# Kernel optimization log

Measured on AMD Instinct MI355X. Metric: run time of the kernel, lower is better.

Reference implementation:

```python
import jax, jax.numpy as jnp
import numpy as np

NU = NI = 100_000  # nodes per ntype
E = 500_000        # edges per metapath graph
M = 2              # metapaths per ntype
D = 64             # in_size == out_size (num_heads = 1)
H = 128            # semantic-attention hidden
B = 8192           # batch of (user, pos, neg) indices
LRELU = 0.2        # DGL GATConv leaky-relu slope
EPS = 1e-5


def setup_inputs() -> dict:
    key = jax.random.key(0)
    ks = iter(jax.random.split(key, 40))
    rn = lambda sh, s=0.1: jax.random.normal(next(ks), sh, jnp.float32) * s
    ri = lambda sh, hi: jax.random.randint(next(ks), sh, 0, hi, jnp.int32)
    return dict(
        user_idx=ri((B,), NU), item_idx=ri((B,), NI), neg_item_idx=ri((B,), NI),
        user_feat=rn((NU, D), 1.0), item_feat=rn((NI, D), 1.0),
        u_src=ri((M, E), NU), u_dst=ri((M, E), NU),
        i_src=ri((M, E), NI), i_dst=ri((M, E), NI),
        u_W=rn((M, D, D)), u_al=rn((M, D)), u_ar=rn((M, D)), u_b=rn((M, D)),
        i_W=rn((M, D, D)), i_al=rn((M, D)), i_ar=rn((M, D)), i_b=rn((M, D)),
        u_saW1=rn((D, H)), u_sab1=rn((H,)), u_saW2=rn((H, 1)),
        i_saW1=rn((D, H)), i_sab1=rn((H,)), i_saW2=rn((H, 1)),
        userW=rn((D, D)), userb=rn((D,)), itemW=rn((D, D)), itemb=rn((D,)),
        ln_g=jnp.ones((D,), jnp.float32), ln_b=jnp.zeros((D,), jnp.float32),
    )


def _gat_stack(h, W, al, ar, b, src, dst, n_nodes):
    # One GATConv (single head) per metapath, vmapped over the metapath axis.
    def one(Wm, alm, arm, bm, s, d):
        feat = h @ Wm                               # (N, D)
        el = feat @ alm                             # (N,)
        er = feat @ arm                             # (N,)
        e = jax.nn.leaky_relu(el[s] + er[d], LRELU)  # (E,)
        m = jax.ops.segment_max(e, d, num_segments=n_nodes)
        ex = jnp.exp(e - m[d])
        den = jax.ops.segment_sum(ex, d, num_segments=n_nodes)
        alpha = ex / (den[d] + 1e-9)                # per-dst edge softmax
        out = jax.ops.segment_sum(alpha[:, None] * feat[s], d, num_segments=n_nodes)
        return jax.nn.elu(out + bm)                 # (N, D)
    return jax.vmap(one)(W, al, ar, b, src, dst)    # (M, N, D)


def _semantic_attention(z, W1, b1, W2):
    # z: (M, N, D) -> (N, D)
    w = jnp.mean(jnp.tanh(jnp.einsum('mnd,dh->mnh', z, W1) + b1) @ W2, axis=1)  # (M, 1)
    beta = jax.nn.softmax(w, axis=0)                 # softmax over metapaths
    return jnp.sum(beta[:, :, None] * z, axis=0)     # (N, D) -- beta (M,1)->(M,1,1)


def _layernorm(x, g, b):
    mu = x.mean(-1, keepdims=True)
    v = ((x - mu) ** 2).mean(-1, keepdims=True)
    return g * (x - mu) / jnp.sqrt(v + EPS) + b


def reference(user_idx, item_idx, neg_item_idx, user_feat, item_feat,
              u_src, u_dst, i_src, i_dst,
              u_W, u_al, u_ar, u_b, i_W, i_al, i_ar, i_b,
              u_saW1, u_sab1, u_saW2, i_saW1, i_sab1, i_saW2,
              userW, userb, itemW, itemb, ln_g, ln_b):
    zu = _gat_stack(user_feat, u_W, u_al, u_ar, u_b, u_src, u_dst, NU)
    zi = _gat_stack(item_feat, i_W, i_al, i_ar, i_b, i_src, i_dst, NI)
    user_emb = _semantic_attention(zu, u_saW1, u_sab1, u_saW2)
    item_emb = _semantic_attention(zi, i_saW1, i_sab1, i_saW2)
    user_emb = _layernorm(jax.nn.relu(user_emb @ userW + userb), ln_g, ln_b)
    item_emb = _layernorm(jax.nn.relu(item_emb @ itemW + itemb), ln_g, ln_b)
    return (user_emb[user_idx], item_emb[item_idx], item_emb[neg_item_idx])
```

## Files before the change

kernel.cpp:

```cpp
#include <hip/hip_runtime.h>
#include <math.h>

#define N_NODES 100000
#define N_EDGES 500000
#define BATCH   8192
#define NBLK    98

typedef __bf16 bf16;
typedef __bf16 bf16x8 __attribute__((ext_vector_type(8)));
typedef float  f32x4  __attribute__((ext_vector_type(4)));

#define MFMA16(a, b, c) __builtin_amdgcn_mfma_f32_16x16x32_bf16((a), (b), (c), 0, 0, 0)

__device__ __forceinline__ float wave_reduce_sum(float v) {
    #pragma unroll
    for (int off = 32; off; off >>= 1) v += __shfl_xor(v, off);
    return v;
}

__device__ __forceinline__ float fast_tanh(float x) {
    float e = __expf(2.f * x);
    return 1.f - 2.f / (e + 1.f);
}

__device__ __forceinline__ float b2f(unsigned short u) {
    return __int_as_float(((int)u) << 16);
}

__global__ void __launch_bounds__(256, 4)
feat_mfma(const float* __restrict__ uf, const float* __restrict__ itf,
          const float* __restrict__ uW, const float* __restrict__ iW,
          const float* __restrict__ ual, const float* __restrict__ ial,
          const float* __restrict__ uar, const float* __restrict__ iar,
          bf16* __restrict__ feat, float* __restrict__ el,
          float* __restrict__ er, int N) {
    const int t = blockIdx.y;
    const float* h   = t ? itf : uf;
    const float* Wb  = t ? iW : uW;
    const float* alb = t ? ial : ual;
    const float* arb = t ? iar : uar;
    __shared__ bf16x8 ldsW[16][64];
    for (int f = threadIdx.x; f < 16 * 64; f += blockDim.x) {
        int id = f >> 6, l = f & 63;
        int lc = l & 15, lq = l >> 4;
        int kf = id & 1, nt = (id >> 1) & 3, m = id >> 3;
        bf16x8 v;
        #pragma unroll
        for (int j = 0; j < 8; ++j)
            v[j] = (bf16)Wb[m * 4096 + (kf * 32 + lq * 8 + j) * 64 + nt * 16 + lc];
        ldsW[id][l] = v;
    }
    __syncthreads();
    const int lane = threadIdx.x & 63, wave = threadIdx.x >> 6, wpb = blockDim.x >> 6;
    const int c = lane & 15, q = lane >> 4;
    float alv[2][4], arv[2][4];
    #pragma unroll
    for (int m = 0; m < 2; ++m)
        #pragma unroll
        for (int nt = 0; nt < 4; ++nt) {
            alv[m][nt] = alb[m * 64 + nt * 16 + c];
            arv[m][nt] = arb[m * 64 + nt * 16 + c];
        }
    const f32x4 zf = {0.f, 0.f, 0.f, 0.f};
    const int tiles = N >> 4;
    for (int tile = blockIdx.x * wpb + wave; tile < tiles; tile += gridDim.x * wpb) {
        const float* hr = h + (size_t)(tile * 16 + c) * 64 + q * 8;
        f32x4 v0 = *(const f32x4*)hr;
        f32x4 v1 = *(const f32x4*)(hr + 4);
        f32x4 v2 = *(const f32x4*)(hr + 32);
        f32x4 v3 = *(const f32x4*)(hr + 36);
        bf16x8 a0, a1;
        #pragma unroll
        for (int j = 0; j < 4; ++j) {
            a0[j] = (bf16)v0[j]; a0[j + 4] = (bf16)v1[j];
            a1[j] = (bf16)v2[j]; a1[j + 4] = (bf16)v3[j];
        }
        #pragma unroll
        for (int m = 0; m < 2; ++m) {
            const int g = t * 2 + m;
            bf16* fg   = feat + (size_t)g * N * 64;
            float* elg = el + (size_t)g * N;
            float* erg = er + (size_t)g * N;
            f32x4 acc[4];
            #pragma unroll
            for (int nt = 0; nt < 4; ++nt) {
                acc[nt] = zf;
                acc[nt] = MFMA16(a0, ldsW[(m * 4 + nt) * 2][lane], acc[nt]);
                acc[nt] = MFMA16(a1, ldsW[(m * 4 + nt) * 2 + 1][lane], acc[nt]);
            }
            #pragma unroll
            for (int nt = 0; nt < 4; ++nt)
                #pragma unroll
                for (int r = 0; r < 4; ++r)
                    fg[(size_t)(tile * 16 + q * 4 + r) * 64 + nt * 16 + c] = (bf16)acc[nt][r];
            #pragma unroll
            for (int r = 0; r < 4; ++r) {
                float se = 0.f, sr = 0.f;
                #pragma unroll
                for (int nt = 0; nt < 4; ++nt) {
                    se = fmaf(acc[nt][r], alv[m][nt], se);
                    sr = fmaf(acc[nt][r], arv[m][nt], sr);
                }
                #pragma unroll
                for (int off = 1; off < 16; off <<= 1) {
                    se += __shfl_xor(se, off);
                    sr += __shfl_xor(sr, off);
                }
                if (c == 0) {
                    elg[tile * 16 + q * 4 + r] = se;
                    erg[tile * 16 + q * 4 + r] = sr;
                }
            }
        }
    }
}

__global__ void hist_all(const int* __restrict__ udst, const int* __restrict__ idst,
                         int* __restrict__ counts, int* __restrict__ rank, int E, int N) {
    const int g = blockIdx.y;
    const int* dst = ((g < 2) ? udst : idst) + (size_t)(g & 1) * E;
    int* cnt = counts + (size_t)g * N;
    int* rk  = rank + (size_t)g * E;
    for (int i = blockIdx.x * blockDim.x + threadIdx.x; i < E; i += gridDim.x * blockDim.x)
        rk[i] = atomicAdd(&cnt[dst[i]], 1);
}

__global__ void scanA(const int* __restrict__ counts, int* __restrict__ offsets,
                      int* __restrict__ bsum, int N) {
    const int g = blockIdx.y;
    const int* c = counts + (size_t)g * N;
    int* o = offsets + (size_t)g * (N + 1);
    __shared__ int sh[1024];
    int i = blockIdx.x * 1024 + (int)threadIdx.x;
    int v = (i < N) ? c[i] : 0;
    sh[threadIdx.x] = v;
    __syncthreads();
    for (int off = 1; off < 1024; off <<= 1) {
        int tv = (threadIdx.x >= (unsigned)off) ? sh[threadIdx.x - off] : 0;
        __syncthreads();
        sh[threadIdx.x] += tv;
        __syncthreads();
    }
    if (i < N) o[i] = sh[threadIdx.x] - v;
    if (threadIdx.x == 1023) bsum[g * 128 + blockIdx.x] = sh[1023];
}

__global__ void scanB(int* __restrict__ bsum, int* __restrict__ offsets, int N) {
    const int g = blockIdx.y;
    int* bs = bsum + g * 128;
    __shared__ int sh[128];
    int tid = (int)threadIdx.x;
    int v = (tid < NBLK) ? bs[tid] : 0;
    sh[tid] = v;
    __syncthreads();
    for (int off = 1; off < 128; off <<= 1) {
        int tv = (tid >= off) ? sh[tid - off] : 0;
        __syncthreads();
        sh[tid] += tv;
        __syncthreads();
    }
    if (tid < NBLK) bs[tid] = sh[tid] - v;
    if (tid == 0) offsets[(size_t)g * (N + 1) + N] = sh[127];
}

__global__ void scanC(int* __restrict__ offsets, const int* __restrict__ bsum, int N) {
    const int g = blockIdx.y;
    int i = blockIdx.x * blockDim.x + threadIdx.x;
    if (i < N)
        offsets[(size_t)g * (N + 1) + i] += bsum[g * 128 + (i >> 10)];
}

__global__ void scatter_all(const int* __restrict__ usrc, const int* __restrict__ udst,
                            const int* __restrict__ isrc, const int* __restrict__ idst,
                            const float* __restrict__ el, const float* __restrict__ er,
                            const int* __restrict__ offsets, const int* __restrict__ rank,
                            int2* __restrict__ epack, int E, int N) {
    const int g = blockIdx.y;
    const int* src = ((g < 2) ? usrc : isrc) + (size_t)(g & 1) * E;
    const int* dst = ((g < 2) ? udst : idst) + (size_t)(g & 1) * E;
    const float* elg = el + (size_t)g * N;
    const float* erg = er + (size_t)g * N;
    const int* offg = offsets + (size_t)g * (N + 1);
    const int* rk = rank + (size_t)g * E;
    int2* ep = epack + (size_t)g * E;
    for (int i = blockIdx.x * blockDim.x + threadIdx.x; i < E; i += gridDim.x * blockDim.x) {
        int s = src[i], d = dst[i];
        int pos = offg[d] + rk[i];
        float e = elg[s] + erg[d];
        e = (e >= 0.f) ? e : 0.2f * e;
        float w = __expf(e);
        ep[pos] = make_int2(s << 7, __float_as_int(w));
    }
}

__global__ void agg_all(const unsigned short* __restrict__ feat,
                        const float* __restrict__ ub, const float* __restrict__ ib,
                        const int* __restrict__ offsets, const int2* __restrict__ epack,
                        bf16* __restrict__ z, int E, int N) {
    const int g = blockIdx.y;
    const char* featg = (const char*)(feat + (size_t)g * N * 64);
    const float* bv = ((g < 2) ? ub : ib) + (g & 1) * 64;
    const int* offg = offsets + (size_t)g * (N + 1);
    const int2* ep = epack + (size_t)g * E;
    bf16* zg = z + (size_t)g * N * 64;
    const int lane = threadIdx.x & 63, wave = threadIdx.x >> 6, wpb = blockDim.x >> 6;
    const int lane2 = lane * 2;
    const float bl = bv[lane];
    for (int node0 = blockIdx.x * wpb + wave; node0 < N; node0 += gridDim.x * wpb) {
        const int node = __builtin_amdgcn_readfirstlane(node0);
        const int beg = __builtin_amdgcn_readfirstlane(offg[node]);
        const int end = __builtin_amdgcn_readfirstlane(offg[node + 1]);
        float l = 0.f, acc0 = 0.f, acc1 = 0.f;
        int i = beg;
        for (; i + 4 <= end; i += 4) {
            int2 p0 = ep[i], p1 = ep[i + 1], p2 = ep[i + 2], p3 = ep[i + 3];
            float f0 = b2f(*(const unsigned short*)(featg + (p0.x + lane2)));
            float f1 = b2f(*(const unsigned short*)(featg + (p1.x + lane2)));
            float f2 = b2f(*(const unsigned short*)(featg + (p2.x + lane2)));
            float f3 = b2f(*(const unsigned short*)(featg + (p3.x + lane2)));
            float w0 = __int_as_float(p0.y), w1 = __int_as_float(p1.y);
            float w2 = __int_as_float(p2.y), w3 = __int_as_float(p3.y);
            l += (w0 + w1) + (w2 + w3);
            acc0 = fmaf(w0, f0, acc0);
            acc1 = fmaf(w1, f1, acc1);
            acc0 = fmaf(w2, f2, acc0);
            acc1 = fmaf(w3, f3, acc1);
        }
        for (; i < end; ++i) {
            int2 p = ep[i];
            float w = __int_as_float(p.y);
            l += w;
            acc0 = fmaf(w, b2f(*(const unsigned short*)(featg + (p.x + lane2))), acc0);
        }
        float acc = acc0 + acc1;
        float o = acc / (l + 1e-9f);
        float zz = o + bl;
        zz = (zz > 0.f) ? zz : expm1f(zz);
        zg[(size_t)node * 64 + lane] = (bf16)zz;
    }
}

__global__ void __launch_bounds__(256, 4)
sem_mfma(const bf16* __restrict__ z,
         const float* __restrict__ uW1, const float* __restrict__ iW1,
         const float* __restrict__ ub1, const float* __restrict__ ib1,
         const float* __restrict__ uW2, const float* __restrict__ iW2,
         float* __restrict__ wsum, int N) {
    const int g = blockIdx.y, t = g >> 1;
    const float* W1 = t ? iW1 : uW1;
    const float* b1 = t ? ib1 : ub1;
    const float* W2 = t ? iW2 : uW2;
    __shared__ bf16x8 ldsW[16][64];
    for (int f = threadIdx.x; f < 16 * 64; f += blockDim.x) {
        int id = f >> 6, l = f & 63;
        int lc = l & 15, lq = l >> 4;
        int nt = id >> 1, kf = id & 1;
        bf16x8 v;
        #pragma unroll
        for (int j = 0; j < 8; ++j)
            v[j] = (bf16)W1[(kf * 32 + lq * 8 + j) * 128 + nt * 16 + lc];
        ldsW[id][l] = v;
    }
    __syncthreads();
    const int lane = threadIdx.x & 63, wave = threadIdx.x >> 6, wpb = blockDim.x >> 6;
    const int c = lane & 15, q = lane >> 4;
    float b1v[8], w2v[8];
    #pragma unroll
    for (int nt = 0; nt < 8; ++nt) { b1v[nt] = b1[nt * 16 + c]; w2v[nt] = W2[nt * 16 + c]; }
    const bf16* zg = z + (size_t)g * N * 64;
    const f32x4 zf = {0.f, 0.f, 0.f, 0.f};
    float local = 0.f;
    const int tiles = N >> 4;
    for (int tile = blockIdx.x * wpb + wave; tile < tiles; tile += gridDim.x * wpb) {
        const bf16* zr = zg + (size_t)(tile * 16 + c) * 64;
        bf16x8 a0 = *(const bf16x8*)(zr + q * 8);
        bf16x8 a1 = *(const bf16x8*)(zr + 32 + q * 8);
        f32x4 acc[8];
        #pragma unroll
        for (int nt = 0; nt < 8; ++nt) {
            acc[nt] = zf;
            acc[nt] = MFMA16(a0, ldsW[nt * 2][lane], acc[nt]);
            acc[nt] = MFMA16(a1, ldsW[nt * 2 + 1][lane], acc[nt]);
        }
        #pragma unroll
        for (int nt = 0; nt < 8; ++nt)
            #pragma unroll
            for (int r = 0; r < 4; ++r)
                local += w2v[nt] * fast_tanh(acc[nt][r] + b1v[nt]);
    }
    local = wave_reduce_sum(local);
    if (lane == 0) atomicAdd(&wsum[g], local);
}

__global__ void out_all(const int* __restrict__ uidx, const int* __restrict__ iidx,
                        const int* __restrict__ nidx, const bf16* __restrict__ z,
                        const float* __restrict__ wsum,
                        const float* __restrict__ userW, const float* __restrict__ userb,
                        const float* __restrict__ itemW, const float* __restrict__ itemb,
                        const float* __restrict__ ln_g, const float* __restrict__ ln_b,
                        float* __restrict__ out, int N, int B) {
    const int grp = blockIdx.y;
    const int t = (grp == 0) ? 0 : 1;
    const float* Wt = t ? itemW : userW;
    const float* bt = t ? itemb : userb;
    const int* idx = (grp == 0) ? uidx : ((grp == 1) ? iidx : nidx);
    const bf16* zg = z + (size_t)(t * 2) * N * 64;
    const int lane = threadIdx.x & 63, wave = threadIdx.x >> 6, wpb = blockDim.x >> 6;
    float Wc[64];
    #pragma unroll
    for (int k = 0; k < 64; ++k) Wc[k] = Wt[k * 64 + lane];
    const float btl = bt[lane], gl = ln_g[lane], lbl = ln_b[lane];
    const float invN = 1.f / (float)N;
    float w0 = wsum[t * 2] * invN, w1 = wsum[t * 2 + 1] * invN;
    float mx = fmaxf(w0, w1);
    float e0 = __expf(w0 - mx), e1 = __expf(w1 - mx);
    float bsum = e0 + e1;
    float beta0 = e0 / bsum, beta1 = e1 / bsum;
    for (int r = blockIdx.x * wpb + wave; r < B; r += gridDim.x * wpb) {
        const int urr = __builtin_amdgcn_readfirstlane(r);
        const int un = __builtin_amdgcn_readfirstlane(idx[urr]);
        float e = beta0 * (float)zg[(size_t)un * 64 + lane]
                + beta1 * (float)zg[(size_t)(N + un) * 64 + lane];
        float y = btl;
        #pragma unroll
        for (int k = 0; k < 64; ++k) y = fmaf(__shfl(e, k), Wc[k], y);
        y = fmaxf(y, 0.f);
        float mu = wave_reduce_sum(y) * (1.f / 64.f);
        float d = y - mu;
        float var = wave_reduce_sum(d * d) * (1.f / 64.f);
        out[(size_t)(grp * B + r) * 64 + lane] = gl * d / sqrtf(var + 1e-5f) + lbl;
    }
}

extern "C" void kernel_launch(void* const* d_in, const int* in_sizes, int n_in,
                              void* d_out, int out_size, void* d_ws, size_t ws_size,
                              hipStream_t stream) {
    const int* user_idx = (const int*)d_in[0];
    const int* item_idx = (const int*)d_in[1];
    const int* neg_idx  = (const int*)d_in[2];
    const float* user_feat = (const float*)d_in[3];
    const float* item_feat = (const float*)d_in[4];
    const int* u_src = (const int*)d_in[5];
    const int* u_dst = (const int*)d_in[6];
    const int* i_src = (const int*)d_in[7];
    const int* i_dst = (const int*)d_in[8];
    const float* u_W  = (const float*)d_in[9];
    const float* u_al = (const float*)d_in[10];
    const float* u_ar = (const float*)d_in[11];
    const float* u_b  = (const float*)d_in[12];
    const float* i_W  = (const float*)d_in[13];
    const float* i_al = (const float*)d_in[14];
    const float* i_ar = (const float*)d_in[15];
    const float* i_b  = (const float*)d_in[16];
    const float* u_saW1 = (const float*)d_in[17];
    const float* u_sab1 = (const float*)d_in[18];
    const float* u_saW2 = (const float*)d_in[19];
    const float* i_saW1 = (const float*)d_in[20];
    const float* i_sab1 = (const float*)d_in[21];
    const float* i_saW2 = (const float*)d_in[22];
    const float* userW = (const float*)d_in[23];
    const float* userb = (const float*)d_in[24];
    const float* itemW = (const float*)d_in[25];
    const float* itemb = (const float*)d_in[26];
    const float* ln_g  = (const float*)d_in[27];
    const float* ln_b  = (const float*)d_in[28];

    const int N = N_NODES, E = N_EDGES, B = BATCH;

    char* ws = (char*)d_ws;
    size_t off = 0;
    auto alloc = [&](size_t bytes) -> char* {
        char* p = ws + off;
        off += (bytes + 255) & ~(size_t)255;
        return p;
    };
    bf16* feat   = (bf16*)alloc((size_t)4 * N * 64 * 2);
    bf16* z      = (bf16*)alloc((size_t)4 * N * 64 * 2);
    float* el    = (float*)alloc((size_t)4 * N * 4);
    float* er    = (float*)alloc((size_t)4 * N * 4);
    int* offsets = (int*)alloc((size_t)4 * (N + 1) * 4);
    int* counts  = (int*)alloc((size_t)4 * N * 4);
    int* rank    = (int*)alloc((size_t)4 * E * 4);
    int2* epack  = (int2*)alloc((size_t)4 * E * 8);
    int* bsum    = (int*)alloc((size_t)4 * 128 * 4);
    float* wsum  = (float*)alloc(16);
    (void)ws_size; (void)in_sizes; (void)n_in; (void)out_size;

    dim3 blk(256);
    hipMemsetAsync(wsum, 0, 16, stream);
    hipMemsetAsync(counts, 0, (size_t)4 * N * 4, stream);

    feat_mfma<<<dim3(256, 2), blk, 0, stream>>>(user_feat, item_feat, u_W, i_W,
                                                u_al, i_al, u_ar, i_ar, feat, el, er, N);
    hist_all<<<dim3(512, 4), blk, 0, stream>>>(u_dst, i_dst, counts, rank, E, N);
    scanA<<<dim3(NBLK, 4), dim3(1024), 0, stream>>>(counts, offsets, bsum, N);
    scanB<<<dim3(1, 4), dim3(128), 0, stream>>>(bsum, offsets, N);
    scanC<<<dim3(391, 4), blk, 0, stream>>>(offsets, bsum, N);
    scatter_all<<<dim3(1024, 4), blk, 0, stream>>>(u_src, u_dst, i_src, i_dst,
                                                   el, er, offsets, rank, epack, E, N);
    agg_all<<<dim3(2048, 4), blk, 0, stream>>>((const unsigned short*)feat, u_b, i_b,
                                               offsets, epack, z, E, N);
    sem_mfma<<<dim3(256, 4), blk, 0, stream>>>(z, u_saW1, i_saW1, u_sab1, i_sab1,
                                               u_saW2, i_saW2, wsum, N);
    out_all<<<dim3(512, 3), blk, 0, stream>>>(user_idx, item_idx, neg_idx, z, wsum,
                                              userW, userb, itemW, itemb, ln_g, ln_b,
                                              (float*)d_out, N, B);
}
```

Measured before the change: 352.5 us.

## Split degree histogram into four sub-counters and aggregate four nodes per wave

The histogram now spreads its atomics over four sub-count arrays chosen by edge index, to reduce atomic contention. The scan sums the four sub-counts, and scanC writes per-node int4 sub-offsets that the scatter uses to place edges. Scatter and histogram are unrolled by four for more loads in flight. Aggregation has each wave handle four consecutive nodes in lockstep up to the largest of their degrees, to expose more independent gathers; the cost is padded iterations and a larger zeroing memset.

Result: slower. 378.1 us (+7.3%).

```diff
diff --git a/kernel.cpp b/kernel.cpp
--- a/kernel.cpp
+++ b/kernel.cpp
@@ -116,23 +116,41 @@
 }
 
 __global__ void hist_all(const int* __restrict__ udst, const int* __restrict__ idst,
-                         int* __restrict__ counts, int* __restrict__ rank, int E, int N) {
+                         int* __restrict__ cnt4, int* __restrict__ rank, int E, int N) {
     const int g = blockIdx.y;
     const int* dst = ((g < 2) ? udst : idst) + (size_t)(g & 1) * E;
-    int* cnt = counts + (size_t)g * N;
-    int* rk  = rank + (size_t)g * E;
-    for (int i = blockIdx.x * blockDim.x + threadIdx.x; i < E; i += gridDim.x * blockDim.x)
-        rk[i] = atomicAdd(&cnt[dst[i]], 1);
-}
-
-__global__ void scanA(const int* __restrict__ counts, int* __restrict__ offsets,
+    int* cntg = cnt4 + (size_t)g * N;
+    int* rk = rank + (size_t)g * E;
+    const int tid = blockIdx.x * blockDim.x + threadIdx.x;
+    const int stride = gridDim.x * blockDim.x;
+    for (int i0 = tid; i0 < E; i0 += 4 * stride) {
+        const int i1 = i0 + stride, i2 = i0 + 2 * stride, i3 = i0 + 3 * stride;
+        int d0 = dst[i0];
+        int d1 = (i1 < E) ? dst[i1] : 0;
+        int d2 = (i2 < E) ? dst[i2] : 0;
+        int d3 = (i3 < E) ? dst[i3] : 0;
+        int r0 = 0, r1 = 0, r2 = 0, r3 = 0;
+        r0 = atomicAdd(&cntg[(size_t)(i0 & 3) * 4 * N + d0], 1);
+        if (i1 < E) r1 = atomicAdd(&cntg[(size_t)(i1 & 3) * 4 * N + d1], 1);
+        if (i2 < E) r2 = atomicAdd(&cntg[(size_t)(i2 & 3) * 4 * N + d2], 1);
+        if (i3 < E) r3 = atomicAdd(&cntg[(size_t)(i3 & 3) * 4 * N + d3], 1);
+        rk[i0] = r0;
+        if (i1 < E) rk[i1] = r1;
+        if (i2 < E) rk[i2] = r2;
+        if (i3 < E) rk[i3] = r3;
+    }
+}
+
+__global__ void scanA(const int* __restrict__ cnt4, int* __restrict__ offsets,
                       int* __restrict__ bsum, int N) {
     const int g = blockIdx.y;
-    const int* c = counts + (size_t)g * N;
+    const int* c = cnt4 + (size_t)g * N;
     int* o = offsets + (size_t)g * (N + 1);
     __shared__ int sh[1024];
     int i = blockIdx.x * 1024 + (int)threadIdx.x;
-    int v = (i < N) ? c[i] : 0;
+    int v = 0;
+    if (i < N)
+        v = c[i] + c[(size_t)4 * N + i] + c[(size_t)8 * N + i] + c[(size_t)12 * N + i];
     sh[threadIdx.x] = v;
     __syncthreads();
     for (int off = 1; off < 1024; off <<= 1) {
@@ -163,33 +181,48 @@
     if (tid == 0) offsets[(size_t)g * (N + 1) + N] = sh[127];
 }
 
-__global__ void scanC(int* __restrict__ offsets, const int* __restrict__ bsum, int N) {
+__global__ void scanC(int* __restrict__ offsets, int* __restrict__ off4,
+                      const int* __restrict__ cnt4, const int* __restrict__ bsum, int N) {
     const int g = blockIdx.y;
     int i = blockIdx.x * blockDim.x + threadIdx.x;
-    if (i < N)
-        offsets[(size_t)g * (N + 1) + i] += bsum[g * 128 + (i >> 10)];
+    if (i < N) {
+        int base = offsets[(size_t)g * (N + 1) + i] + bsum[g * 128 + (i >> 10)];
+        offsets[(size_t)g * (N + 1) + i] = base;
+        const int* c = cnt4 + (size_t)g * N;
+        int c0 = c[i], c1 = c[(size_t)4 * N + i], c2 = c[(size_t)8 * N + i];
+        int4 o;
+        o.x = base; o.y = base + c0; o.z = base + c0 + c1; o.w = base + c0 + c1 + c2;
+        *(int4*)(off4 + ((size_t)g * N + i) * 4) = o;
+    }
 }
 
 __global__ void scatter_all(const int* __restrict__ usrc, const int* __restrict__ udst,
                             const int* __restrict__ isrc, const int* __restrict__ idst,
                             const float* __restrict__ el, const float* __restrict__ er,
-                            const int* __restrict__ offsets, const int* __restrict__ rank,
+                            const int* __restrict__ off4, const int* __restrict__ rank,
                             int2* __restrict__ epack, int E, int N) {
     const int g = blockIdx.y;
     const int* src = ((g < 2) ? usrc : isrc) + (size_t)(g & 1) * E;
     const int* dst = ((g < 2) ? udst : idst) + (size_t)(g & 1) * E;
     const float* elg = el + (size_t)g * N;
     const float* erg = er + (size_t)g * N;
-    const int* offg = offsets + (size_t)g * (N + 1);
+    const int* o4 = off4 + (size_t)g * N * 4;
     const int* rk = rank + (size_t)g * E;
     int2* ep = epack + (size_t)g * E;
-    for (int i = blockIdx.x * blockDim.x + threadIdx.x; i < E; i += gridDim.x * blockDim.x) {
-        int s = src[i], d = dst[i];
-        int pos = offg[d] + rk[i];
-        float e = elg[s] + erg[d];
-        e = (e >= 0.f) ? e : 0.2f * e;
-        float w = __expf(e);
-        ep[pos] = make_int2(s << 7, __float_as_int(w));
+    const int tid = blockIdx.x * blockDim.x + threadIdx.x;
+    const int stride = gridDim.x * blockDim.x;
+    for (int i0 = tid; i0 < E; i0 += 4 * stride) {
+        #pragma unroll
+        for (int u = 0; u < 4; ++u) {
+            const int i = i0 + u * stride;
+            if (i < E) {
+                int s = src[i], d = dst[i];
+                int pos = o4[d * 4 + (i & 3)] + rk[i];
+                float e = elg[s] + erg[d];
+                e = (e >= 0.f) ? e : 0.2f * e;
+                ep[pos] = make_int2(s << 7, __float_as_int(__expf(e)));
+            }
+        }
     }
 }
 
@@ -206,37 +239,61 @@
     const int lane = threadIdx.x & 63, wave = threadIdx.x >> 6, wpb = blockDim.x >> 6;
     const int lane2 = lane * 2;
     const float bl = bv[lane];
-    for (int node0 = blockIdx.x * wpb + wave; node0 < N; node0 += gridDim.x * wpb) {
-        const int node = __builtin_amdgcn_readfirstlane(node0);
-        const int beg = __builtin_amdgcn_readfirstlane(offg[node]);
-        const int end = __builtin_amdgcn_readfirstlane(offg[node + 1]);
-        float l = 0.f, acc0 = 0.f, acc1 = 0.f;
-        int i = beg;
-        for (; i + 4 <= end; i += 4) {
-            int2 p0 = ep[i], p1 = ep[i + 1], p2 = ep[i + 2], p3 = ep[i + 3];
-            float f0 = b2f(*(const unsigned short*)(featg + (p0.x + lane2)));
-            float f1 = b2f(*(const unsigned short*)(featg + (p1.x + lane2)));
-            float f2 = b2f(*(const unsigned short*)(featg + (p2.x + lane2)));
-            float f3 = b2f(*(const unsigned short*)(featg + (p3.x + lane2)));
-            float w0 = __int_as_float(p0.y), w1 = __int_as_float(p1.y);
-            float w2 = __int_as_float(p2.y), w3 = __int_as_float(p3.y);
-            l += (w0 + w1) + (w2 + w3);
-            acc0 = fmaf(w0, f0, acc0);
-            acc1 = fmaf(w1, f1, acc1);
-            acc0 = fmaf(w2, f2, acc0);
-            acc1 = fmaf(w3, f3, acc1);
-        }
-        for (; i < end; ++i) {
-            int2 p = ep[i];
-            float w = __int_as_float(p.y);
-            l += w;
-            acc0 = fmaf(w, b2f(*(const unsigned short*)(featg + (p.x + lane2))), acc0);
-        }
-        float acc = acc0 + acc1;
-        float o = acc / (l + 1e-9f);
-        float zz = o + bl;
-        zz = (zz > 0.f) ? zz : expm1f(zz);
-        zg[(size_t)node * 64 + lane] = (bf16)zz;
+    const int nquad = N >> 2;
+    for (int quad = blockIdx.x * wpb + wave; quad < nquad; quad += gridDim.x * wpb) {
+        const int n0 = __builtin_amdgcn_readfirstlane(quad << 2);
+        const int o0 = __builtin_amdgcn_readfirstlane(offg[n0]);
+        const int o1 = __builtin_amdgcn_readfirstlane(offg[n0 + 1]);
+        const int o2 = __builtin_amdgcn_readfirstlane(offg[n0 + 2]);
+        const int o3 = __builtin_amdgcn_readfirstlane(offg[n0 + 3]);
+        const int o4_ = __builtin_amdgcn_readfirstlane(offg[n0 + 4]);
+        const int d0 = o1 - o0, d1 = o2 - o1, d2 = o3 - o2, d3 = o4_ - o3;
+        int maxd = max(max(d0, d1), max(d2, d3));
+        float l0 = 0.f, l1 = 0.f, l2 = 0.f, l3 = 0.f;
+        float a0 = 0.f, a1 = 0.f, a2 = 0.f, a3 = 0.f;
+        for (int s = 0; s < maxd; s += 2) {
+            const int sA = s, sB = s + 1;
+            int2 pA0 = ep[(sA < d0) ? o0 + sA : 0];
+            int2 pA1 = ep[(sA < d1) ? o1 + sA : 0];
+            int2 pA2 = ep[(sA < d2) ? o2 + sA : 0];
+            int2 pA3 = ep[(sA < d3) ? o3 + sA : 0];
+            int2 pB0 = ep[(sB < d0) ? o0 + sB : 0];
+            int2 pB1 = ep[(sB < d1) ? o1 + sB : 0];
+            int2 pB2 = ep[(sB < d2) ? o2 + sB : 0];
+            int2 pB3 = ep[(sB < d3) ? o3 + sB : 0];
+            float fA0 = b2f(*(const unsigned short*)(featg + (pA0.x + lane2)));
+            float fA1 = b2f(*(const unsigned short*)(featg + (pA1.x + lane2)));
+            float fA2 = b2f(*(const unsigned short*)(featg + (pA2.x + lane2)));
+            float fA3 = b2f(*(const unsigned short*)(featg + (pA3.x + lane2)));
+            float fB0 = b2f(*(const unsigned short*)(featg + (pB0.x + lane2)));
+            float fB1 = b2f(*(const unsigned short*)(featg + (pB1.x + lane2)));
+            float fB2 = b2f(*(const unsigned short*)(featg + (pB2.x + lane2)));
+            float fB3 = b2f(*(const unsigned short*)(featg + (pB3.x + lane2)));
+            float wA0 = (sA < d0) ? __int_as_float(pA0.y) : 0.f;
+            float wA1 = (sA < d1) ? __int_as_float(pA1.y) : 0.f;
+            float wA2 = (sA < d2) ? __int_as_float(pA2.y) : 0.f;
+            float wA3 = (sA < d3) ? __int_as_float(pA3.y) : 0.f;
+            float wB0 = (sB < d0) ? __int_as_float(pB0.y) : 0.f;
+            float wB1 = (sB < d1) ? __int_as_float(pB1.y) : 0.f;
+            float wB2 = (sB < d2) ? __int_as_float(pB2.y) : 0.f;
+            float wB3 = (sB < d3) ? __int_as_float(pB3.y) : 0.f;
+            l0 += wA0 + wB0; l1 += wA1 + wB1; l2 += wA2 + wB2; l3 += wA3 + wB3;
+            a0 = fmaf(wA0, fA0, a0); a0 = fmaf(wB0, fB0, a0);
+            a1 = fmaf(wA1, fA1, a1); a1 = fmaf(wB1, fB1, a1);
+            a2 = fmaf(wA2, fA2, a2); a2 = fmaf(wB2, fB2, a2);
+            a3 = fmaf(wA3, fA3, a3); a3 = fmaf(wB3, fB3, a3);
+        }
+        float oo0 = a0 / (l0 + 1e-9f), oo1 = a1 / (l1 + 1e-9f);
+        float oo2 = a2 / (l2 + 1e-9f), oo3 = a3 / (l3 + 1e-9f);
+        float z0 = oo0 + bl, z1 = oo1 + bl, z2 = oo2 + bl, z3 = oo3 + bl;
+        z0 = (z0 > 0.f) ? z0 : expm1f(z0);
+        z1 = (z1 > 0.f) ? z1 : expm1f(z1);
+        z2 = (z2 > 0.f) ? z2 : expm1f(z2);
+        z3 = (z3 > 0.f) ? z3 : expm1f(z3);
+        zg[(size_t)(n0 + 0) * 64 + lane] = (bf16)z0;
+        zg[(size_t)(n0 + 1) * 64 + lane] = (bf16)z1;
+        zg[(size_t)(n0 + 2) * 64 + lane] = (bf16)z2;
+        zg[(size_t)(n0 + 3) * 64 + lane] = (bf16)z3;
     }
 }
 
@@ -379,7 +436,8 @@
     float* el    = (float*)alloc((size_t)4 * N * 4);
     float* er    = (float*)alloc((size_t)4 * N * 4);
     int* offsets = (int*)alloc((size_t)4 * (N + 1) * 4);
-    int* counts  = (int*)alloc((size_t)4 * N * 4);
+    int* cnt4    = (int*)alloc((size_t)16 * N * 4);
+    int* off4    = (int*)alloc((size_t)4 * N * 4 * 4);
     int* rank    = (int*)alloc((size_t)4 * E * 4);
     int2* epack  = (int2*)alloc((size_t)4 * E * 8);
     int* bsum    = (int*)alloc((size_t)4 * 128 * 4);
@@ -388,17 +446,17 @@
 
     dim3 blk(256);
     hipMemsetAsync(wsum, 0, 16, stream);
-    hipMemsetAsync(counts, 0, (size_t)4 * N * 4, stream);
+    hipMemsetAsync(cnt4, 0, (size_t)16 * N * 4, stream);
 
     feat_mfma<<<dim3(256, 2), blk, 0, stream>>>(user_feat, item_feat, u_W, i_W,
                                                 u_al, i_al, u_ar, i_ar, feat, el, er, N);
-    hist_all<<<dim3(512, 4), blk, 0, stream>>>(u_dst, i_dst, counts, rank, E, N);
-    scanA<<<dim3(NBLK, 4), dim3(1024), 0, stream>>>(counts, offsets, bsum, N);
+    hist_all<<<dim3(512, 4), blk, 0, stream>>>(u_dst, i_dst, cnt4, rank, E, N);
+    scanA<<<dim3(NBLK, 4), dim3(1024), 0, stream>>>(cnt4, offsets, bsum, N);
     scanB<<<dim3(1, 4), dim3(128), 0, stream>>>(bsum, offsets, N);
-    scanC<<<dim3(391, 4), blk, 0, stream>>>(offsets, bsum, N);
-    scatter_all<<<dim3(1024, 4), blk, 0, stream>>>(u_src, u_dst, i_src, i_dst,
-                                                   el, er, offsets, rank, epack, E, N);
-    agg_all<<<dim3(2048, 4), blk, 0, stream>>>((const unsigned short*)feat, u_b, i_b,
+    scanC<<<dim3(391, 4), blk, 0, stream>>>(offsets, off4, cnt4, bsum, N);
+    scatter_all<<<dim3(512, 4), blk, 0, stream>>>(u_src, u_dst, i_src, i_dst,
+                                                  el, er, off4, rank, epack, E, N);
+    agg_all<<<dim3(6250, 4), blk, 0, stream>>>((const unsigned short*)feat, u_b, i_b,
                                                offsets, epack, z, E, N);
     sem_mfma<<<dim3(256, 4), blk, 0, stream>>>(z, u_saW1, i_saW1, u_sab1, i_sab1,
                                                u_saW2, i_saW2, wsum, N);
```

## Split per-destination histogram counters into four sub-counters to reduce atomic contention

Applied to the files above, without the earlier changes.

Replaces the single per-node edge counter with four sub-counters selected by edge index mod 4, and unrolls the histogram and scatter loops by four. scanA sums the sub-counters, and scanC emits per-sub-counter base offsets that scatter uses to place edges. This is meant to reduce atomic contention and raise memory-level parallelism in the CSR build. In exchange it adds a 4x larger memset, extra scan reads and an off4 table write, and scatter gathers from a wider table.

Result: slower. 373.2 us (+5.9%).

```diff
diff --git a/kernel.cpp b/kernel.cpp
--- a/kernel.cpp
+++ b/kernel.cpp
@@ -116,23 +116,41 @@
 }
 
 __global__ void hist_all(const int* __restrict__ udst, const int* __restrict__ idst,
-                         int* __restrict__ counts, int* __restrict__ rank, int E, int N) {
+                         int* __restrict__ cnt4, int* __restrict__ rank, int E, int N) {
     const int g = blockIdx.y;
     const int* dst = ((g < 2) ? udst : idst) + (size_t)(g & 1) * E;
-    int* cnt = counts + (size_t)g * N;
-    int* rk  = rank + (size_t)g * E;
-    for (int i = blockIdx.x * blockDim.x + threadIdx.x; i < E; i += gridDim.x * blockDim.x)
-        rk[i] = atomicAdd(&cnt[dst[i]], 1);
-}
-
-__global__ void scanA(const int* __restrict__ counts, int* __restrict__ offsets,
+    int* cntg = cnt4 + (size_t)g * N;
+    int* rk = rank + (size_t)g * E;
+    const int tid = blockIdx.x * blockDim.x + threadIdx.x;
+    const int stride = gridDim.x * blockDim.x;
+    for (int i0 = tid; i0 < E; i0 += 4 * stride) {
+        const int i1 = i0 + stride, i2 = i0 + 2 * stride, i3 = i0 + 3 * stride;
+        int d0 = dst[i0];
+        int d1 = (i1 < E) ? dst[i1] : 0;
+        int d2 = (i2 < E) ? dst[i2] : 0;
+        int d3 = (i3 < E) ? dst[i3] : 0;
+        int r0 = 0, r1 = 0, r2 = 0, r3 = 0;
+        r0 = atomicAdd(&cntg[(size_t)(i0 & 3) * 4 * N + d0], 1);
+        if (i1 < E) r1 = atomicAdd(&cntg[(size_t)(i1 & 3) * 4 * N + d1], 1);
+        if (i2 < E) r2 = atomicAdd(&cntg[(size_t)(i2 & 3) * 4 * N + d2], 1);
+        if (i3 < E) r3 = atomicAdd(&cntg[(size_t)(i3 & 3) * 4 * N + d3], 1);
+        rk[i0] = r0;
+        if (i1 < E) rk[i1] = r1;
+        if (i2 < E) rk[i2] = r2;
+        if (i3 < E) rk[i3] = r3;
+    }
+}
+
+__global__ void scanA(const int* __restrict__ cnt4, int* __restrict__ offsets,
                       int* __restrict__ bsum, int N) {
     const int g = blockIdx.y;
-    const int* c = counts + (size_t)g * N;
+    const int* c = cnt4 + (size_t)g * N;
     int* o = offsets + (size_t)g * (N + 1);
     __shared__ int sh[1024];
     int i = blockIdx.x * 1024 + (int)threadIdx.x;
-    int v = (i < N) ? c[i] : 0;
+    int v = 0;
+    if (i < N)
+        v = c[i] + c[(size_t)4 * N + i] + c[(size_t)8 * N + i] + c[(size_t)12 * N + i];
     sh[threadIdx.x] = v;
     __syncthreads();
     for (int off = 1; off < 1024; off <<= 1) {
@@ -163,33 +181,48 @@
     if (tid == 0) offsets[(size_t)g * (N + 1) + N] = sh[127];
 }
 
-__global__ void scanC(int* __restrict__ offsets, const int* __restrict__ bsum, int N) {
+__global__ void scanC(int* __restrict__ offsets, int* __restrict__ off4,
+                      const int* __restrict__ cnt4, const int* __restrict__ bsum, int N) {
     const int g = blockIdx.y;
     int i = blockIdx.x * blockDim.x + threadIdx.x;
-    if (i < N)
-        offsets[(size_t)g * (N + 1) + i] += bsum[g * 128 + (i >> 10)];
+    if (i < N) {
+        int base = offsets[(size_t)g * (N + 1) + i] + bsum[g * 128 + (i >> 10)];
+        offsets[(size_t)g * (N + 1) + i] = base;
+        const int* c = cnt4 + (size_t)g * N;
+        int c0 = c[i], c1 = c[(size_t)4 * N + i], c2 = c[(size_t)8 * N + i];
+        int4 o;
+        o.x = base; o.y = base + c0; o.z = base + c0 + c1; o.w = base + c0 + c1 + c2;
+        *(int4*)(off4 + ((size_t)g * N + i) * 4) = o;
+    }
 }
 
 __global__ void scatter_all(const int* __restrict__ usrc, const int* __restrict__ udst,
                             const int* __restrict__ isrc, const int* __restrict__ idst,
                             const float* __restrict__ el, const float* __restrict__ er,
-                            const int* __restrict__ offsets, const int* __restrict__ rank,
+                            const int* __restrict__ off4, const int* __restrict__ rank,
                             int2* __restrict__ epack, int E, int N) {
     const int g = blockIdx.y;
     const int* src = ((g < 2) ? usrc : isrc) + (size_t)(g & 1) * E;
     const int* dst = ((g < 2) ? udst : idst) + (size_t)(g & 1) * E;
     const float* elg = el + (size_t)g * N;
     const float* erg = er + (size_t)g * N;
-    const int* offg = offsets + (size_t)g * (N + 1);
+    const int* o4 = off4 + (size_t)g * N * 4;
     const int* rk = rank + (size_t)g * E;
     int2* ep = epack + (size_t)g * E;
-    for (int i = blockIdx.x * blockDim.x + threadIdx.x; i < E; i += gridDim.x * blockDim.x) {
-        int s = src[i], d = dst[i];
-        int pos = offg[d] + rk[i];
-        float e = elg[s] + erg[d];
-        e = (e >= 0.f) ? e : 0.2f * e;
-        float w = __expf(e);
-        ep[pos] = make_int2(s << 7, __float_as_int(w));
+    const int tid = blockIdx.x * blockDim.x + threadIdx.x;
+    const int stride = gridDim.x * blockDim.x;
+    for (int i0 = tid; i0 < E; i0 += 4 * stride) {
+        #pragma unroll
+        for (int u = 0; u < 4; ++u) {
+            const int i = i0 + u * stride;
+            if (i < E) {
+                int s = src[i], d = dst[i];
+                int pos = o4[d * 4 + (i & 3)] + rk[i];
+                float e = elg[s] + erg[d];
+                e = (e >= 0.f) ? e : 0.2f * e;
+                ep[pos] = make_int2(s << 7, __float_as_int(__expf(e)));
+            }
+        }
     }
 }
 
@@ -379,7 +412,8 @@
     float* el    = (float*)alloc((size_t)4 * N * 4);
     float* er    = (float*)alloc((size_t)4 * N * 4);
     int* offsets = (int*)alloc((size_t)4 * (N + 1) * 4);
-    int* counts  = (int*)alloc((size_t)4 * N * 4);
+    int* cnt4    = (int*)alloc((size_t)16 * N * 4);
+    int* off4    = (int*)alloc((size_t)4 * N * 4 * 4);
     int* rank    = (int*)alloc((size_t)4 * E * 4);
     int2* epack  = (int2*)alloc((size_t)4 * E * 8);
     int* bsum    = (int*)alloc((size_t)4 * 128 * 4);
@@ -388,16 +422,16 @@
 
     dim3 blk(256);
     hipMemsetAsync(wsum, 0, 16, stream);
-    hipMemsetAsync(counts, 0, (size_t)4 * N * 4, stream);
+    hipMemsetAsync(cnt4, 0, (size_t)16 * N * 4, stream);
 
     feat_mfma<<<dim3(256, 2), blk, 0, stream>>>(user_feat, item_feat, u_W, i_W,
                                                 u_al, i_al, u_ar, i_ar, feat, el, er, N);
-    hist_all<<<dim3(512, 4), blk, 0, stream>>>(u_dst, i_dst, counts, rank, E, N);
-    scanA<<<dim3(NBLK, 4), dim3(1024), 0, stream>>>(counts, offsets, bsum, N);
+    hist_all<<<dim3(512, 4), blk, 0, stream>>>(u_dst, i_dst, cnt4, rank, E, N);
+    scanA<<<dim3(NBLK, 4), dim3(1024), 0, stream>>>(cnt4, offsets, bsum, N);
     scanB<<<dim3(1, 4), dim3(128), 0, stream>>>(bsum, offsets, N);
-    scanC<<<dim3(391, 4), blk, 0, stream>>>(offsets, bsum, N);
+    scanC<<<dim3(391, 4), blk, 0, stream>>>(offsets, off4, cnt4, bsum, N);
     scatter_all<<<dim3(1024, 4), blk, 0, stream>>>(u_src, u_dst, i_src, i_dst,
-                                                   el, er, offsets, rank, epack, E, N);
+                                                   el, er, off4, rank, epack, E, N);
     agg_all<<<dim3(2048, 4), blk, 0, stream>>>((const unsigned short*)feat, u_b, i_b,
                                                offsets, epack, z, E, N);
     sem_mfma<<<dim3(256, 4), blk, 0, stream>>>(z, u_saW1, i_saW1, u_sab1, i_sab1,
```
